# Kernel optimization log

Measured on AMD Instinct MI355X. Metric: run time of the kernel, lower is better.

Reference implementation:

```python
import math
import jax, jax.numpy as jnp
import numpy as np

D_MODEL = 256
NUM_HEAD = 8
NUM_LEVEL = 1
KERNEL = 5
NUM_POINT = KERNEL * KERNEL
NUM_VAR = 5  # with_rotation=True
HEAD_DIM = D_MODEL // NUM_HEAD


def _kernel_indices(k=KERNEL):
    # odd kernel: linspace(-(k-1)/2, (k-1)/2, k); torch.meshgrid default 'ij'; stack([j,i])/k
    idx = jnp.linspace(-(k - 1) / 2.0, (k - 1) / 2.0, k)
    ii, jj = jnp.meshgrid(idx, idx, indexing='ij')
    return jnp.stack([jj, ii], axis=-1).reshape(-1, 2) / k  # (P, 2)


def setup_inputs() -> dict:
    key = jax.random.key(0)
    ks = jax.random.split(key, 8)
    B, LQ = 2, 4096
    Hf, Wf = 188, 188
    LV = Hf * Wf
    d = D_MODEL
    nb = NUM_LEVEL * NUM_HEAD * NUM_VAR
    na = NUM_HEAD * NUM_LEVEL * NUM_POINT
    return {
        'query': jax.random.normal(ks[0], (B, LQ, d), jnp.float32),
        'value': jax.random.normal(ks[1], (B, LV, d), jnp.float32),
        'ref_windows': jax.random.uniform(ks[2], (B, LQ, 7), jnp.float32),
        'W_box': jax.random.normal(ks[3], (nb, d), jnp.float32) * 0.02,
        'b_box': jax.random.uniform(ks[4], (nb,), jnp.float32),
        'W_attn': jax.random.normal(ks[5], (na, d), jnp.float32) * 0.02,
        'b_attn': jnp.zeros((na,), jnp.float32),
        'W_value': jax.random.normal(ks[6], (d, d), jnp.float32) * 0.02,
        'b_value': jnp.zeros((d,), jnp.float32),
        'W_out': jax.random.normal(ks[7], (d, d), jnp.float32) * 0.02,
        'b_out': jnp.zeros((d,), jnp.float32),
        'H_feat': Hf,
        'W_feat': Wf,
    }


def reference(query, value, ref_windows, W_box, b_box, W_attn, b_attn,
              W_value, b_value, W_out, b_out, H_feat, W_feat):
    B, LQ, d = query.shape
    LV = value.shape[1]
    Hh, Lv, P, Dh = NUM_HEAD, NUM_LEVEL, NUM_POINT, HEAD_DIM

    # value projection -> (B, LV, Hh, Dh)
    v = (value @ W_value.T + b_value).reshape(B, LV, Hh, Dh)

    # attention weights: softmax over (level*point) per head
    attn = jax.nn.softmax((query @ W_attn.T + b_attn).reshape(B, LQ, Hh, Lv * P), axis=-1)
    attn = attn.reshape(B, LQ, Hh, Lv, P)

    # --- _where_to_attend ---
    ob = (query @ W_box.T + b_box).reshape(B, LQ, Hh, Lv, NUM_VAR)
    rw = ref_windows[:, :, None, None, :]                    # (B,LQ,1,1,7)
    ref_boxes = rw[..., jnp.array([0, 1, 3, 4])]             # cx, cy, w, h
    ref_angles = rw[..., 6:7]
    off_boxes, off_angles = ob[..., :4], ob[..., 4:5]
    angles = (ref_angles + off_angles / 16.0) * (2.0 * math.pi)
    boxes = ref_boxes + off_boxes / 8.0 * ref_boxes[..., jnp.array([2, 3, 2, 3])]
    center = boxes[..., None, :2]                            # (B,LQ,Hh,Lv,1,2)
    size = boxes[..., None, 2:4]
    cos_a, sin_a = jnp.cos(angles), jnp.sin(angles)
    rot = jnp.stack([cos_a, -sin_a, sin_a, cos_a], axis=-1).reshape(B, LQ, Hh, Lv, 1, 2, 2)
    g = _kernel_indices() * jax.nn.relu(size)                # (B,LQ,Hh,Lv,P,2)
    grid = center + (g[..., None, :] * rot).sum(-1)          # (B,LQ,Hh,Lv,P,2), normalized [0,1]

    # --- single-level bilinear sampling (align_corners=False, zero padding) ---
    gl = grid[:, :, :, 0]                                    # (B,LQ,Hh,P,2)
    gx = gl[..., 0] * W_feat - 0.5
    gy = gl[..., 1] * H_feat - 0.5
    x0 = jnp.floor(gx)
    y0 = jnp.floor(gy)
    x0i = x0.astype(jnp.int32)
    y0i = y0.astype(jnp.int32)
    wx1 = gx - x0
    wy1 = gy - y0
    wx0 = 1.0 - wx1
    wy0 = 1.0 - wy1

    b_idx = jnp.arange(B)[:, None, None, None]
    h_idx = jnp.arange(Hh)[None, None, :, None]

    def gather(yi, xi):
        valid = (xi >= 0) & (xi < W_feat) & (yi >= 0) & (yi < H_feat)
        lin = jnp.clip(yi, 0, H_feat - 1) * W_feat + jnp.clip(xi, 0, W_feat - 1)
        return v[b_idx, lin, h_idx] * valid[..., None]       # (B,LQ,Hh,P,Dh)

    s = (gather(y0i, x0i) * (wy0 * wx0)[..., None]
         + gather(y0i, x0i + 1) * (wy0 * wx1)[..., None]
         + gather(y0i + 1, x0i) * (wy1 * wx0)[..., None]
         + gather(y0i + 1, x0i + 1) * (wy1 * wx1)[..., None])

    out_heads = (s * attn[:, :, :, 0, :, None]).sum(axis=3)  # (B,LQ,Hh,Dh)
    out = out_heads.reshape(B, LQ, Hh * Dh) @ W_out.T + b_out
    attn_w = attn.reshape(B, LQ, Hh, Lv, KERNEL, KERNEL)
    return out, attn_w
```

## Files before the change

kernel.cpp:

```cpp
#include <hip/hip_runtime.h>


typedef float floatx4 __attribute__((ext_vector_type(4)));
typedef short shortx8 __attribute__((ext_vector_type(8)));

#define SB0 __builtin_amdgcn_sched_barrier(0)
#define VMCNT8 asm volatile("s_waitcnt vmcnt(8)" ::: "memory")
#define VMCNT0 asm volatile("s_waitcnt vmcnt(0)" ::: "memory")
#define LGKM0  asm volatile("s_waitcnt lgkmcnt(0)" ::: "memory")

static __device__ __forceinline__ unsigned short f2bf(float x) {
    unsigned int u = __float_as_uint(x);
    return (unsigned short)((u + 0x7fffu + ((u >> 16) & 1u)) >> 16);
}
static __device__ __forceinline__ unsigned int pack2(float a, float b) {
    return (unsigned int)f2bf(a) | ((unsigned int)f2bf(b) << 16);
}
static __device__ __forceinline__ void async16(const void* g, void* lds) {
    __builtin_amdgcn_global_load_lds(
        (const __attribute__((address_space(1))) unsigned int*)g,
        (__attribute__((address_space(3))) unsigned int*)lds, 16, 0, 0);
}

__global__ __launch_bounds__(256) void convert_kernel(
    const float* __restrict__ W_value, unsigned short* __restrict__ wvbf,
    const float* __restrict__ W_attn, const float* __restrict__ W_box,
    float* __restrict__ Wab,
    const float* __restrict__ W_out, unsigned short* __restrict__ wobf,
    const float* __restrict__ b_attn, const float* __restrict__ b_box,
    float* __restrict__ bab)
{
    const int blk = blockIdx.x, tid = threadIdx.x;
    if (blk < 16) {
        int base = blk * 1024 + tid;
#pragma unroll
        for (int k = 0; k < 4; ++k) {
            int j = base + k * 256;
            float4 f = ((const float4*)W_value)[j];
            ((uint2*)wvbf)[j] = make_uint2(pack2(f.x, f.y), pack2(f.z, f.w));
        }
    } else if (blk < 32) {
        int base = (blk - 16) * 1024 + tid;
#pragma unroll
        for (int k = 0; k < 4; ++k) {
            int j = base + k * 256;
            int row = j >> 6, col = (j & 63) * 4;
            float4 f;
            if (row < 200)      f = *(const float4*)(W_attn + (size_t)row * 256 + col);
            else if (row < 240) f = *(const float4*)(W_box + (size_t)(row - 200) * 256 + col);
            else                f = make_float4(0.f, 0.f, 0.f, 0.f);
            ((float4*)Wab)[j] = f;
        }
    } else if (blk < 48) {
        int base = (blk - 32) * 1024 + tid;
#pragma unroll
        for (int k = 0; k < 4; ++k) {
            int j = base + k * 256;
            float4 f = ((const float4*)W_out)[j];
            ((uint2*)wobf)[j] = make_uint2(pack2(f.x, f.y), pack2(f.z, f.w));
        }
    } else {
        bab[tid] = tid < 200 ? b_attn[tid] : (tid < 240 ? b_box[tid - 200] : 0.f);
    }
}

template <int OUTMODE, int AFP32, int BM>
__global__ __launch_bounds__(256) void gemm_bf16(
    const void* __restrict__ Av,
    const unsigned short* __restrict__ Bw,
    const float* __restrict__ bias,
    void* __restrict__ Cv, int M, int LV)
{
    constexpr int NI = BM / 32;
    constexpr int TI = BM / 32;
    __shared__ unsigned short As[2][BM * 64];
    __shared__ unsigned short Bs[2][128 * 64];
    const int tid = threadIdx.x;
    const int wv = tid >> 6, lane = tid & 63;
    const int lr = lane & 15, lq = lane >> 4;
    const int m0 = blockIdx.x * BM, n0 = blockIdx.y * 128;
    const int wm = wv & 1, wn = wv >> 1;
    const int srow = tid >> 3;
    const int colg = tid & 7;
    const int colgSw = colg ^ (srow & 7);
    const int dstA = (srow * 8 + colgSw) * 16;

    floatx4 acc[TI][4];
#pragma unroll
    for (int i = 0; i < TI; ++i)
#pragma unroll
        for (int j = 0; j < 4; ++j) acc[i][j] = (floatx4){0.f, 0.f, 0.f, 0.f};

    auto compute = [&](const unsigned short* Acur, const unsigned short* Bcur) {
#pragma unroll
        for (int kb = 0; kb < 2; ++kb) {
            shortx8 af[TI], bfr[4];
#pragma unroll
            for (int t = 0; t < TI; ++t) {
                int arow = wm * (BM / 2) + t * 16 + lr;
                af[t] = *(const shortx8*)&Acur[arow * 64 + (((kb * 4 + lq) ^ (arow & 7)) * 8)];
            }
#pragma unroll
            for (int t = 0; t < 4; ++t) {
                int brow = wn * 64 + t * 16 + lr;
                bfr[t] = *(const shortx8*)&Bcur[brow * 64 + (((kb * 4 + lq) ^ (brow & 7)) * 8)];
            }
#pragma unroll
            for (int ti = 0; ti < TI; ++ti)
#pragma unroll
                for (int tj = 0; tj < 4; ++tj)
                    acc[ti][tj] = __builtin_amdgcn_mfma_f32_16x16x32_bf16(bfr[tj], af[ti], acc[ti][tj], 0, 0, 0);
        }
    };

    if constexpr (AFP32) {
        const float* Af = (const float*)Av;
        const float* aptr[NI];
#pragma unroll
        for (int i = 0; i < NI; ++i) {
            int ra = m0 + i * 32 + srow; ra = ra < M ? ra : M - 1;
            aptr[i] = Af + (size_t)ra * 256 + colg * 8;
        }
        const unsigned short* bptr = Bw + (size_t)(n0 + srow) * 256 + colgSw * 8;
        float4 ar0[NI], ar1[NI];

#pragma unroll
        for (int i = 0; i < NI; ++i) { ar0[i] = *(const float4*)aptr[i]; ar1[i] = *(const float4*)(aptr[i] + 4); }
#pragma unroll
        for (int i = 0; i < 4; ++i)
            async16(bptr + (size_t)i * 8192, (char*)Bs[0] + i * 4096 + wv * 1024);
        SB0;
#pragma unroll
        for (int i = 0; i < NI; ++i) {
            uint4 pv = make_uint4(pack2(ar0[i].x, ar0[i].y), pack2(ar0[i].z, ar0[i].w),
                                  pack2(ar1[i].x, ar1[i].y), pack2(ar1[i].z, ar1[i].w));
            *(uint4*)((char*)As[0] + i * 4096 + dstA) = pv;
        }
#pragma unroll
        for (int i = 0; i < NI; ++i) { ar0[i] = *(const float4*)(aptr[i] + 64); ar1[i] = *(const float4*)(aptr[i] + 68); }
        SB0;
        VMCNT8;
        LGKM0;
        __builtin_amdgcn_s_barrier();
        SB0;

#pragma unroll
        for (int kc = 0; kc < 4; ++kc) {
            const int cur = kc & 1;
            if (kc < 3) {
#pragma unroll
                for (int i = 0; i < 4; ++i)
                    async16(bptr + (size_t)i * 8192 + (kc + 1) * 64,
                            (char*)Bs[cur ^ 1] + i * 4096 + wv * 1024);
            }
            SB0;
            compute(As[cur], Bs[cur]);
            SB0;
            if (kc < 3) {
#pragma unroll
                for (int i = 0; i < NI; ++i) {
                    uint4 pv = make_uint4(pack2(ar0[i].x, ar0[i].y), pack2(ar0[i].z, ar0[i].w),
                                          pack2(ar1[i].x, ar1[i].y), pack2(ar1[i].z, ar1[i].w));
                    *(uint4*)((char*)As[cur ^ 1] + i * 4096 + dstA) = pv;
                }
                if (kc < 2) {
#pragma unroll
                    for (int i = 0; i < NI; ++i) {
                        ar0[i] = *(const float4*)(aptr[i] + (kc + 2) * 64);
                        ar1[i] = *(const float4*)(aptr[i] + (kc + 2) * 64 + 4);
                    }
                    SB0;
                    VMCNT8;
                } else {
                    SB0;
                    VMCNT0;
                }
                LGKM0;
                __builtin_amdgcn_s_barrier();
                SB0;
            }
        }
    } else {
        const unsigned short* Ab = (const unsigned short*)Av;
#pragma unroll
        for (int i = 0; i < NI; ++i) {
            int ra = m0 + i * 32 + srow; ra = ra < M ? ra : M - 1;
            async16(Ab + (size_t)ra * 256 + colgSw * 8, (char*)As[0] + i * 4096 + wv * 1024);
        }
#pragma unroll
        for (int i = 0; i < 4; ++i) {
            int rb = n0 + i * 32 + srow;
            async16(Bw + (size_t)rb * 256 + colgSw * 8, (char*)Bs[0] + i * 4096 + wv * 1024);
        }
        __syncthreads();
        int cur = 0;
        for (int kc = 0; kc < 4; ++kc) {
            const int nk = (kc + 1) * 64;
            if (kc < 3) {
#pragma unroll
                for (int i = 0; i < NI; ++i) {
                    int ra = m0 + i * 32 + srow; ra = ra < M ? ra : M - 1;
                    async16(Ab + (size_t)ra * 256 + nk + colgSw * 8,
                            (char*)As[cur ^ 1] + i * 4096 + wv * 1024);
                }
#pragma unroll
                for (int i = 0; i < 4; ++i) {
                    int rb = n0 + i * 32 + srow;
                    async16(Bw + (size_t)rb * 256 + nk + colgSw * 8,
                            (char*)Bs[cur ^ 1] + i * 4096 + wv * 1024);
                }
            }
            compute(As[cur], Bs[cur]);
            __syncthreads();
            cur ^= 1;
        }
    }

#pragma unroll
    for (int ti = 0; ti < TI; ++ti) {
        int m = m0 + wm * (BM / 2) + ti * 16 + lr;
        if (m >= M) continue;
        if (OUTMODE == 0) {
            float* Crow = (float*)Cv + (size_t)m * 256;
#pragma unroll
            for (int tj = 0; tj < 4; ++tj) {
                int nb = n0 + wn * 64 + tj * 16 + lq * 4;
                float4 bv = *(const float4*)(bias + nb);
                float4 o = make_float4(acc[ti][tj][0] + bv.x, acc[ti][tj][1] + bv.y,
                                       acc[ti][tj][2] + bv.z, acc[ti][tj][3] + bv.w);
                *(float4*)(Crow + nb) = o;
            }
        } else {
            int b = m >= LV ? 1 : 0;
            int lv = m - (b ? LV : 0);
#pragma unroll
            for (int tj = 0; tj < 4; ++tj) {
                int nb = n0 + wn * 64 + tj * 16 + lq * 4;
                float4 bv = *(const float4*)(bias + nb);
                int h = nb >> 5, dh = nb & 31;
                unsigned short* dst = (unsigned short*)Cv + ((size_t)(b * 8 + h) * LV + lv) * 32 + dh;
                *(uint2*)dst = make_uint2(pack2(acc[ti][tj][0] + bv.x, acc[ti][tj][1] + bv.y),
                                          pack2(acc[ti][tj][2] + bv.z, acc[ti][tj][3] + bv.w));
            }
        }
    }
}

__global__ __launch_bounds__(256) void gemm_nt_bias(
    const float* __restrict__ A, const float* __restrict__ W,
    const float* __restrict__ bias, float* __restrict__ C, int M)
{
    const int K = 256, N = 256;
    __shared__ float As[16][68];
    __shared__ float Bs[16][68];
    int tid = threadIdx.x;
    int tcol = tid & 15, trow = tid >> 4;
    int m0 = blockIdx.x * 64, n0 = blockIdx.y * 64;
    int lr = tid >> 2, lc = (tid & 3) << 2;
    float acc[4][4] = {};
    for (int k0 = 0; k0 < K; k0 += 16) {
        int arow = m0 + lr; if (arow > M - 1) arow = M - 1;
        float4 av = *(const float4*)(A + (size_t)arow * K + k0 + lc);
        float4 wv = *(const float4*)(W + (size_t)(n0 + lr) * K + k0 + lc);
        __syncthreads();
        As[lc + 0][lr] = av.x; As[lc + 1][lr] = av.y; As[lc + 2][lr] = av.z; As[lc + 3][lr] = av.w;
        Bs[lc + 0][lr] = wv.x; Bs[lc + 1][lr] = wv.y; Bs[lc + 2][lr] = wv.z; Bs[lc + 3][lr] = wv.w;
        __syncthreads();
#pragma unroll
        for (int k = 0; k < 16; ++k) {
            float4 a4 = *(const float4*)&As[k][trow << 2];
            float4 b4 = *(const float4*)&Bs[k][tcol << 2];
            float a[4] = {a4.x, a4.y, a4.z, a4.w};
            float bb[4] = {b4.x, b4.y, b4.z, b4.w};
#pragma unroll
            for (int i = 0; i < 4; i++)
#pragma unroll
                for (int j = 0; j < 4; j++) acc[i][j] += a[i] * bb[j];
        }
    }
#pragma unroll
    for (int i = 0; i < 4; i++) {
        int m = m0 + trow * 4 + i;
        if (m >= M) continue;
#pragma unroll
        for (int j = 0; j < 4; j++) {
            int n = n0 + tcol * 4 + j;
            C[(size_t)m * N + n] = acc[i][j] + bias[n];
        }
    }
}

__global__ __launch_bounds__(256) void decode_sample_kernel(
    const unsigned short* __restrict__ v,
    const float* __restrict__ logits,
    const float* __restrict__ ref_windows,
    float* __restrict__ attn_out,
    unsigned short* __restrict__ ohbf,
    const int* __restrict__ Hf_p, const int* __restrict__ Wf_p, int LV, int LQ)
{
    __shared__ float lg[8][32];
    __shared__ float rw[8][7];
    __shared__ float prm[8][6];
    __shared__ float mxinv[8][2];
    __shared__ uint4 pk[8][25][2];

    const int lin = blockIdx.y * 16 + blockIdx.x;
    const int nc = gridDim.y;
    const int seq = lin >> 3;
    const int c = seq % nc;
    const int s = (lin & 7) + ((seq / nc) << 3);
    const int b = s >> 3, h = s & 7;
    const int tid = threadIdx.x;
    const int Hf = *Hf_p, Wf = *Wf_p;
    const size_t mbase = (size_t)b * LQ + c * 8;

    if (tid < 240) {
        int qq = tid / 30, j = tid - qq * 30;
        int col = (j < 25) ? h * 25 + j : 200 + h * 5 + (j - 25);
        lg[qq][j] = logits[(mbase + qq) * 256 + col];
    }
    if (tid < 56) {
        int qq = tid / 7, k = tid - qq * 7;
        rw[qq][k] = ref_windows[(mbase + qq) * 7 + k];
    }
    __syncthreads();

    if (tid < 8) {
        int qq = tid;
        float mx = -1e30f;
#pragma unroll
        for (int p = 0; p < 25; p++) mx = fmaxf(mx, lg[qq][p]);
        float ssum = 0.f;
#pragma unroll
        for (int p = 0; p < 25; p++) ssum += expf(lg[qq][p] - mx);
        mxinv[qq][0] = mx; mxinv[qq][1] = 1.f / ssum;
        float cx = rw[qq][0] + lg[qq][25] * 0.125f * rw[qq][3];
        float cy = rw[qq][1] + lg[qq][26] * 0.125f * rw[qq][4];
        float bw = rw[qq][3] + lg[qq][27] * 0.125f * rw[qq][3];
        float bh = rw[qq][4] + lg[qq][28] * 0.125f * rw[qq][4];
        float ang = (rw[qq][6] + lg[qq][29] * 0.0625f) * 6.283185307179586f;
        prm[qq][0] = cx; prm[qq][1] = cy;
        prm[qq][2] = fmaxf(bw, 0.f); prm[qq][3] = fmaxf(bh, 0.f);
        prm[qq][4] = cosf(ang); prm[qq][5] = sinf(ang);
    }
    __syncthreads();

    if (tid < 200) {
        int qq = tid / 25, p = tid - qq * 25;
        float a = expf(lg[qq][p] - mxinv[qq][0]) * mxinv[qq][1];
        attn_out[(mbase + qq) * 200 + h * 25 + p] = a;
        int pi = p / 5, pj = p - pi * 5;
        float g0 = (float)(pj - 2) * 0.2f * prm[qq][2];
        float g1 = (float)(pi - 2) * 0.2f * prm[qq][3];
        float ca = prm[qq][4], sa = prm[qq][5];
        float gx = (prm[qq][0] + g0 * ca - g1 * sa) * (float)Wf - 0.5f;
        float gy = (prm[qq][1] + g0 * sa + g1 * ca) * (float)Hf - 0.5f;
        float x0f = floorf(gx), y0f = floorf(gy);
        int x0 = (int)x0f, y0 = (int)y0f;
        float wx1 = gx - x0f, wy1 = gy - y0f;
        float wx0 = 1.f - wx1, wy0 = 1.f - wy1;
        int y1 = y0 + 1;
        int bx; float wl, wr;
        if (x0 >= 0 && x0 <= Wf - 2)      { bx = x0;     wl = wx0; wr = wx1; }
        else if (x0 == -1)                { bx = 0;      wl = wx1; wr = 0.f; }
        else if (x0 == Wf - 1)            { bx = Wf - 2; wl = 0.f; wr = wx0; }
        else                              { bx = 0;      wl = 0.f; wr = 0.f; }
        float wy0v = (y0 >= 0 && y0 < Hf) ? wy0 : 0.f;
        float wy1v = (y1 >= 0 && y1 < Hf) ? wy1 : 0.f;
        int cy0 = min(max(y0, 0), Hf - 1), cy1 = min(max(y1, 0), Hf - 1);
        unsigned off0 = (unsigned)(cy0 * Wf + bx) * 16u;
        unsigned off1 = (unsigned)(cy1 * Wf + bx) * 16u;
        float aw0 = a * wy0v, aw1 = a * wy1v;
        pk[qq][p][0] = make_uint4(__float_as_uint(aw0 * wl), __float_as_uint(aw1 * wl), off0, off1);
        pk[qq][p][1] = make_uint4(__float_as_uint(aw0 * wr), __float_as_uint(aw1 * wr), off0, off1);
    }
    __syncthreads();

    const int qq = tid >> 5, l = tid & 31;
    const unsigned int* vw = (const unsigned int*)(v + (size_t)s * LV * 32);
    const uint4* pkp = &pk[qq][0][l >> 4];
    float e0 = 0.f, o0 = 0.f, e1 = 0.f, o1 = 0.f;
#pragma unroll
    for (int p = 0; p < 25; ++p) {
        uint4 t = pkp[2 * p];
        float w0 = __uint_as_float(t.x), w1 = __uint_as_float(t.y);
        unsigned u0 = vw[t.z + l];
        unsigned u1 = vw[t.w + l];
        e0 += w0 * __uint_as_float(u0 << 16);
        o0 += w0 * __uint_as_float(u0 & 0xffff0000u);
        e1 += w1 * __uint_as_float(u1 << 16);
        o1 += w1 * __uint_as_float(u1 & 0xffff0000u);
    }
    float a0 = e0 + e1, a1 = o0 + o1;
    a0 += __shfl_xor(a0, 16, 32);
    a1 += __shfl_xor(a1, 16, 32);
    if (l < 16)
        ((unsigned int*)ohbf)[(mbase + qq) * 128 + h * 16 + l] = pack2(a0, a1);
}

extern "C" void kernel_launch(void* const* d_in, const int* in_sizes, int n_in,
                              void* d_out, int out_size, void* d_ws, size_t ws_size,
                              hipStream_t stream) {
    const float* query       = (const float*)d_in[0];
    const float* value       = (const float*)d_in[1];
    const float* ref_windows = (const float*)d_in[2];
    const float* W_box       = (const float*)d_in[3];
    const float* b_box       = (const float*)d_in[4];
    const float* W_attn      = (const float*)d_in[5];
    const float* b_attn      = (const float*)d_in[6];
    const float* W_value     = (const float*)d_in[7];
    const float* b_value     = (const float*)d_in[8];
    const float* W_out       = (const float*)d_in[9];
    const float* b_out       = (const float*)d_in[10];
    const int*   Hf          = (const int*)d_in[11];
    const int*   Wf          = (const int*)d_in[12];

    const int M1 = in_sizes[1] / 256;
    const int MQ = in_sizes[0] / 256;
    const int LQ = MQ / 2;
    const int LV = M1 / 2;

    unsigned short* Vout = (unsigned short*)d_ws;
    unsigned short* ohbf = Vout + (size_t)M1 * 256;
    unsigned short* wvbf = ohbf + (size_t)MQ * 256;
    unsigned short* wobf = wvbf + 65536;
    float* Wab       = (float*)(wobf + 65536);
    float* bab       = Wab + 65536;
    float* logits    = bab + 256;

    float* out0     = (float*)d_out;
    float* attn_out = out0 + (size_t)MQ * 256;

    convert_kernel<<<49, 256, 0, stream>>>(W_value, wvbf, W_attn, W_box, Wab,
                                           W_out, wobf, b_attn, b_box, bab);
    dim3 g1((M1 + 127) / 128, 2);
    gemm_bf16<1, 1, 128><<<g1, 256, 0, stream>>>(value, wvbf, b_value, Vout, M1, LV);
    dim3 g2(MQ / 64, 4);
    gemm_nt_bias<<<g2, 256, 0, stream>>>(query, Wab, bab, logits, MQ);
    decode_sample_kernel<<<dim3(16, LQ / 8), 256, 0, stream>>>(
        Vout, logits, ref_windows, attn_out, ohbf, Hf, Wf, LV, LQ);
    dim3 g4(MQ / 64, 2);
    gemm_bf16<0, 0, 64><<<g4, 256, 0, stream>>>(ohbf, wobf, b_out, out0, MQ, LV);
}
```

Measured before the change: 212.4 us.

## Fuse value and query projection GEMMs into one interleaved launch

```diff
diff --git a/kernel.cpp b/kernel.cpp
--- a/kernel.cpp
+++ b/kernel.cpp
@@ -64,80 +64,87 @@
     }
 }
 
-template <int OUTMODE, int AFP32, int BM>
-__global__ __launch_bounds__(256) void gemm_bf16(
-    const void* __restrict__ Av,
-    const unsigned short* __restrict__ Bw,
-    const float* __restrict__ bias,
-    void* __restrict__ Cv, int M, int LV)
+__global__ __launch_bounds__(256) void fused_proj(
+    const float* __restrict__ value,
+    const unsigned short* __restrict__ wvbf,
+    const float* __restrict__ b_value,
+    unsigned short* __restrict__ Vout, int M1, int LV,
+    const float* __restrict__ query,
+    const float* __restrict__ Wab,
+    const float* __restrict__ bab,
+    float* __restrict__ logits, int MQ)
 {
-    constexpr int NI = BM / 32;
-    constexpr int TI = BM / 32;
-    __shared__ unsigned short As[2][BM * 64];
-    __shared__ unsigned short Bs[2][128 * 64];
+    __shared__ char smem[65536];
+    const int f = blockIdx.x;
     const int tid = threadIdx.x;
-    const int wv = tid >> 6, lane = tid & 63;
-    const int lr = lane & 15, lq = lane >> 4;
-    const int m0 = blockIdx.x * BM, n0 = blockIdx.y * 128;
-    const int wm = wv & 1, wn = wv >> 1;
-    const int srow = tid >> 3;
-    const int colg = tid & 7;
-    const int colgSw = colg ^ (srow & 7);
-    const int dstA = (srow * 8 + colgSw) * 16;
-
-    floatx4 acc[TI][4];
-#pragma unroll
-    for (int i = 0; i < TI; ++i)
-#pragma unroll
-        for (int j = 0; j < 4; ++j) acc[i][j] = (floatx4){0.f, 0.f, 0.f, 0.f};
-
-    auto compute = [&](const unsigned short* Acur, const unsigned short* Bcur) {
-#pragma unroll
-        for (int kb = 0; kb < 2; ++kb) {
-            shortx8 af[TI], bfr[4];
-#pragma unroll
-            for (int t = 0; t < TI; ++t) {
-                int arow = wm * (BM / 2) + t * 16 + lr;
-                af[t] = *(const shortx8*)&Acur[arow * 64 + (((kb * 4 + lq) ^ (arow & 7)) * 8)];
-            }
-#pragma unroll
-            for (int t = 0; t < 4; ++t) {
-                int brow = wn * 64 + t * 16 + lr;
-                bfr[t] = *(const shortx8*)&Bcur[brow * 64 + (((kb * 4 + lq) ^ (brow & 7)) * 8)];
-            }
-#pragma unroll
-            for (int ti = 0; ti < TI; ++ti)
-#pragma unroll
-                for (int tj = 0; tj < 4; ++tj)
-                    acc[ti][tj] = __builtin_amdgcn_mfma_f32_16x16x32_bf16(bfr[tj], af[ti], acc[ti][tj], 0, 0, 0);
-        }
-    };
-
-    if constexpr (AFP32) {
-        const float* Af = (const float*)Av;
-        const float* aptr[NI];
-#pragma unroll
-        for (int i = 0; i < NI; ++i) {
+    const bool isK2 = (f % 3 == 2) && (f < 1536);
+
+    if (!isK2) {
+        const int k1id = f - ((f < 1536) ? ((f + 1) / 3) : 512);
+        const int bx = k1id % 553, by = k1id / 553;
+        unsigned short* AsL = (unsigned short*)smem;
+        unsigned short* BsL = (unsigned short*)smem + 16384;
+        const int wv = tid >> 6, lane = tid & 63;
+        const int lr = lane & 15, lq = lane >> 4;
+        const int m0 = bx * 128, n0 = by * 128;
+        const int wm = wv & 1, wn = wv >> 1;
+        const int srow = tid >> 3;
+        const int colg = tid & 7;
+        const int colgSw = colg ^ (srow & 7);
+        const int dstA = (srow * 8 + colgSw) * 16;
+        const int M = M1;
+
+        floatx4 acc[4][4];
+#pragma unroll
+        for (int i = 0; i < 4; ++i)
+#pragma unroll
+            for (int j = 0; j < 4; ++j) acc[i][j] = (floatx4){0.f, 0.f, 0.f, 0.f};
+
+        auto compute = [&](const unsigned short* Acur, const unsigned short* Bcur) {
+#pragma unroll
+            for (int kb = 0; kb < 2; ++kb) {
+                shortx8 af[4], bfr[4];
+#pragma unroll
+                for (int t = 0; t < 4; ++t) {
+                    int arow = wm * 64 + t * 16 + lr;
+                    af[t] = *(const shortx8*)&Acur[arow * 64 + (((kb * 4 + lq) ^ (arow & 7)) * 8)];
+                }
+#pragma unroll
+                for (int t = 0; t < 4; ++t) {
+                    int brow = wn * 64 + t * 16 + lr;
+                    bfr[t] = *(const shortx8*)&Bcur[brow * 64 + (((kb * 4 + lq) ^ (brow & 7)) * 8)];
+                }
+#pragma unroll
+                for (int ti = 0; ti < 4; ++ti)
+#pragma unroll
+                    for (int tj = 0; tj < 4; ++tj)
+                        acc[ti][tj] = __builtin_amdgcn_mfma_f32_16x16x32_bf16(bfr[tj], af[ti], acc[ti][tj], 0, 0, 0);
+            }
+        };
+
+        const float* aptr[4];
+#pragma unroll
+        for (int i = 0; i < 4; ++i) {
             int ra = m0 + i * 32 + srow; ra = ra < M ? ra : M - 1;
-            aptr[i] = Af + (size_t)ra * 256 + colg * 8;
-        }
-        const unsigned short* bptr = Bw + (size_t)(n0 + srow) * 256 + colgSw * 8;
-        float4 ar0[NI], ar1[NI];
-
-#pragma unroll
-        for (int i = 0; i < NI; ++i) { ar0[i] = *(const float4*)aptr[i]; ar1[i] = *(const float4*)(aptr[i] + 4); }
+            aptr[i] = value + (size_t)ra * 256 + colg * 8;
+        }
+        const unsigned short* bptr = wvbf + (size_t)(n0 + srow) * 256 + colgSw * 8;
+        float4 ar0[4], ar1[4];
+
+#pragma unroll
+        for (int i = 0; i < 4; ++i) { ar0[i] = *(const float4*)aptr[i]; ar1[i] = *(const float4*)(aptr[i] + 4); }
 #pragma unroll
         for (int i = 0; i < 4; ++i)
-            async16(bptr + (size_t)i * 8192, (char*)Bs[0] + i * 4096 + wv * 1024);
+            async16(bptr + (size_t)i * 8192, (char*)BsL + i * 4096 + wv * 1024);
         SB0;
 #pragma unroll
-        for (int i = 0; i < NI; ++i) {
+        for (int i = 0; i < 4; ++i) {
             uint4 pv = make_uint4(pack2(ar0[i].x, ar0[i].y), pack2(ar0[i].z, ar0[i].w),
                                   pack2(ar1[i].x, ar1[i].y), pack2(ar1[i].z, ar1[i].w));
-            *(uint4*)((char*)As[0] + i * 4096 + dstA) = pv;
-        }
-#pragma unroll
-        for (int i = 0; i < NI; ++i) { ar0[i] = *(const float4*)(aptr[i] + 64); ar1[i] = *(const float4*)(aptr[i] + 68); }
+            *(uint4*)((char*)AsL + i * 4096 + dstA) = pv;
+        }
+#pragma unroll
+        for (int i = 0; i < 4; ++i) { ar0[i] = *(const float4*)(aptr[i] + 64); ar1[i] = *(const float4*)(aptr[i] + 68); }
         SB0;
         VMCNT8;
         LGKM0;
@@ -147,25 +154,29 @@
 #pragma unroll
         for (int kc = 0; kc < 4; ++kc) {
             const int cur = kc & 1;
+            unsigned short* Acur = AsL + cur * 8192;
+            unsigned short* Anxt = AsL + (cur ^ 1) * 8192;
+            unsigned short* Bcur = BsL + cur * 8192;
+            unsigned short* Bnxt = BsL + (cur ^ 1) * 8192;
             if (kc < 3) {
 #pragma unroll
                 for (int i = 0; i < 4; ++i)
                     async16(bptr + (size_t)i * 8192 + (kc + 1) * 64,
-                            (char*)Bs[cur ^ 1] + i * 4096 + wv * 1024);
+                            (char*)Bnxt + i * 4096 + wv * 1024);
             }
             SB0;
-            compute(As[cur], Bs[cur]);
+            compute(Acur, Bcur);
             SB0;
             if (kc < 3) {
 #pragma unroll
-                for (int i = 0; i < NI; ++i) {
+                for (int i = 0; i < 4; ++i) {
                     uint4 pv = make_uint4(pack2(ar0[i].x, ar0[i].y), pack2(ar0[i].z, ar0[i].w),
                                           pack2(ar1[i].x, ar1[i].y), pack2(ar1[i].z, ar1[i].w));
-                    *(uint4*)((char*)As[cur ^ 1] + i * 4096 + dstA) = pv;
+                    *(uint4*)((char*)Anxt + i * 4096 + dstA) = pv;
                 }
                 if (kc < 2) {
 #pragma unroll
-                    for (int i = 0; i < NI; ++i) {
+                    for (int i = 0; i < 4; ++i) {
                         ar0[i] = *(const float4*)(aptr[i] + (kc + 2) * 64);
                         ar1[i] = *(const float4*)(aptr[i] + (kc + 2) * 64 + 4);
                     }
@@ -180,112 +191,157 @@
                 SB0;
             }
         }
+#pragma unroll
+        for (int ti = 0; ti < 4; ++ti) {
+            int m = m0 + wm * 64 + ti * 16 + lr;
+            if (m >= M) continue;
+            int b = m >= LV ? 1 : 0;
+            int lv = m - (b ? LV : 0);
+#pragma unroll
+            for (int tj = 0; tj < 4; ++tj) {
+                int nb = n0 + wn * 64 + tj * 16 + lq * 4;
+                float4 bv = *(const float4*)(b_value + nb);
+                int h = nb >> 5, dh = nb & 31;
+                unsigned short* dst = Vout + ((size_t)(b * 8 + h) * LV + lv) * 32 + dh;
+                *(uint2*)dst = make_uint2(pack2(acc[ti][tj][0] + bv.x, acc[ti][tj][1] + bv.y),
+                                          pack2(acc[ti][tj][2] + bv.z, acc[ti][tj][3] + bv.w));
+            }
+        }
     } else {
-        const unsigned short* Ab = (const unsigned short*)Av;
-#pragma unroll
-        for (int i = 0; i < NI; ++i) {
-            int ra = m0 + i * 32 + srow; ra = ra < M ? ra : M - 1;
-            async16(Ab + (size_t)ra * 256 + colgSw * 8, (char*)As[0] + i * 4096 + wv * 1024);
-        }
-#pragma unroll
-        for (int i = 0; i < 4; ++i) {
-            int rb = n0 + i * 32 + srow;
-            async16(Bw + (size_t)rb * 256 + colgSw * 8, (char*)Bs[0] + i * 4096 + wv * 1024);
-        }
+        const int id = f / 3;
+        const int m0 = (id & 127) * 64, n0 = (id >> 7) * 64;
+        const int K = 256, N = 256, M = MQ;
+        float* As2 = (float*)smem;
+        float* Bs2 = (float*)smem + 16 * 68;
+        int tcol = tid & 15, trow = tid >> 4;
+        int lr = tid >> 2, lc = (tid & 3) << 2;
+        float acc[4][4] = {};
+        for (int k0 = 0; k0 < K; k0 += 16) {
+            int arow = m0 + lr; if (arow > M - 1) arow = M - 1;
+            float4 av = *(const float4*)(query + (size_t)arow * K + k0 + lc);
+            float4 wv = *(const float4*)(Wab + (size_t)(n0 + lr) * K + k0 + lc);
+            __syncthreads();
+            As2[(lc + 0) * 68 + lr] = av.x; As2[(lc + 1) * 68 + lr] = av.y;
+            As2[(lc + 2) * 68 + lr] = av.z; As2[(lc + 3) * 68 + lr] = av.w;
+            Bs2[(lc + 0) * 68 + lr] = wv.x; Bs2[(lc + 1) * 68 + lr] = wv.y;
+            Bs2[(lc + 2) * 68 + lr] = wv.z; Bs2[(lc + 3) * 68 + lr] = wv.w;
+            __syncthreads();
+#pragma unroll
+            for (int k = 0; k < 16; ++k) {
+                float4 a4 = *(const float4*)&As2[k * 68 + (trow << 2)];
+                float4 b4 = *(const float4*)&Bs2[k * 68 + (tcol << 2)];
+                float a[4] = {a4.x, a4.y, a4.z, a4.w};
+                float bb[4] = {b4.x, b4.y, b4.z, b4.w};
+#pragma unroll
+                for (int i = 0; i < 4; i++)
+#pragma unroll
+                    for (int j = 0; j < 4; j++) acc[i][j] += a[i] * bb[j];
+            }
+        }
+#pragma unroll
+        for (int i = 0; i < 4; i++) {
+            int m = m0 + trow * 4 + i;
+            if (m >= M) continue;
+#pragma unroll
+            for (int j = 0; j < 4; j++) {
+                int n = n0 + tcol * 4 + j;
+                logits[(size_t)m * N + n] = acc[i][j] + bab[n];
+            }
+        }
+    }
+}
+
+__global__ __launch_bounds__(256) void gemm_out(
+    const unsigned short* __restrict__ Ab,
+    const unsigned short* __restrict__ Bw,
+    const float* __restrict__ bias,
+    float* __restrict__ C, int M)
+{
+    constexpr int BM = 64;
+    constexpr int NI = BM / 32, TI = BM / 32;
+    __shared__ unsigned short As[2][BM * 64];
+    __shared__ unsigned short Bs[2][128 * 64];
+    const int tid = threadIdx.x;
+    const int wv = tid >> 6, lane = tid & 63;
+    const int lr = lane & 15, lq = lane >> 4;
+    const int m0 = blockIdx.x * BM, n0 = blockIdx.y * 128;
+    const int wm = wv & 1, wn = wv >> 1;
+    const int srow = tid >> 3;
+    const int colg = tid & 7;
+    const int colgSw = colg ^ (srow & 7);
+
+    floatx4 acc[TI][4];
+#pragma unroll
+    for (int i = 0; i < TI; ++i)
+#pragma unroll
+        for (int j = 0; j < 4; ++j) acc[i][j] = (floatx4){0.f, 0.f, 0.f, 0.f};
+
+    auto compute = [&](const unsigned short* Acur, const unsigned short* Bcur) {
+#pragma unroll
+        for (int kb = 0; kb < 2; ++kb) {
+            shortx8 af[TI], bfr[4];
+#pragma unroll
+            for (int t = 0; t < TI; ++t) {
+                int arow = wm * (BM / 2) + t * 16 + lr;
+                af[t] = *(const shortx8*)&Acur[arow * 64 + (((kb * 4 + lq) ^ (arow & 7)) * 8)];
+            }
+#pragma unroll
+            for (int t = 0; t < 4; ++t) {
+                int brow = wn * 64 + t * 16 + lr;
+                bfr[t] = *(const shortx8*)&Bcur[brow * 64 + (((kb * 4 + lq) ^ (brow & 7)) * 8)];
+            }
+#pragma unroll
+            for (int ti = 0; ti < TI; ++ti)
+#pragma unroll
+                for (int tj = 0; tj < 4; ++tj)
+                    acc[ti][tj] = __builtin_amdgcn_mfma_f32_16x16x32_bf16(bfr[tj], af[ti], acc[ti][tj], 0, 0, 0);
+        }
+    };
+
+#pragma unroll
+    for (int i = 0; i < NI; ++i) {
+        int ra = m0 + i * 32 + srow; ra = ra < M ? ra : M - 1;
+        async16(Ab + (size_t)ra * 256 + colgSw * 8, (char*)As[0] + i * 4096 + wv * 1024);
+    }
+#pragma unroll
+    for (int i = 0; i < 4; ++i) {
+        int rb = n0 + i * 32 + srow;
+        async16(Bw + (size_t)rb * 256 + colgSw * 8, (char*)Bs[0] + i * 4096 + wv * 1024);
+    }
+    __syncthreads();
+    int cur = 0;
+    for (int kc = 0; kc < 4; ++kc) {
+        const int nk = (kc + 1) * 64;
+        if (kc < 3) {
+#pragma unroll
+            for (int i = 0; i < NI; ++i) {
+                int ra = m0 + i * 32 + srow; ra = ra < M ? ra : M - 1;
+                async16(Ab + (size_t)ra * 256 + nk + colgSw * 8,
+                        (char*)As[cur ^ 1] + i * 4096 + wv * 1024);
+            }
+#pragma unroll
+            for (int i = 0; i < 4; ++i) {
+                int rb = n0 + i * 32 + srow;
+                async16(Bw + (size_t)rb * 256 + nk + colgSw * 8,
+                        (char*)Bs[cur ^ 1] + i * 4096 + wv * 1024);
+            }
+        }
+        compute(As[cur], Bs[cur]);
         __syncthreads();
-        int cur = 0;
-        for (int kc = 0; kc < 4; ++kc) {
-            const int nk = (kc + 1) * 64;
-            if (kc < 3) {
-#pragma unroll
-                for (int i = 0; i < NI; ++i) {
-                    int ra = m0 + i * 32 + srow; ra = ra < M ? ra : M - 1;
-                    async16(Ab + (size_t)ra * 256 + nk + colgSw * 8,
-                            (char*)As[cur ^ 1] + i * 4096 + wv * 1024);
-                }
-#pragma unroll
-                for (int i = 0; i < 4; ++i) {
-                    int rb = n0 + i * 32 + srow;
-                    async16(Bw + (size_t)rb * 256 + nk + colgSw * 8,
-                            (char*)Bs[cur ^ 1] + i * 4096 + wv * 1024);
-                }
-            }
-            compute(As[cur], Bs[cur]);
-            __syncthreads();
-            cur ^= 1;
-        }
-    }
-
+        cur ^= 1;
+    }
 #pragma unroll
     for (int ti = 0; ti < TI; ++ti) {
         int m = m0 + wm * (BM / 2) + ti * 16 + lr;
         if (m >= M) continue;
-        if (OUTMODE == 0) {
-            float* Crow = (float*)Cv + (size_t)m * 256;
-#pragma unroll
-            for (int tj = 0; tj < 4; ++tj) {
-                int nb = n0 + wn * 64 + tj * 16 + lq * 4;
-                float4 bv = *(const float4*)(bias + nb);
-                float4 o = make_float4(acc[ti][tj][0] + bv.x, acc[ti][tj][1] + bv.y,
-                                       acc[ti][tj][2] + bv.z, acc[ti][tj][3] + bv.w);
-                *(float4*)(Crow + nb) = o;
-            }
-        } else {
-            int b = m >= LV ? 1 : 0;
-            int lv = m - (b ? LV : 0);
-#pragma unroll
-            for (int tj = 0; tj < 4; ++tj) {
-                int nb = n0 + wn * 64 + tj * 16 + lq * 4;
-                float4 bv = *(const float4*)(bias + nb);
-                int h = nb >> 5, dh = nb & 31;
-                unsigned short* dst = (unsigned short*)Cv + ((size_t)(b * 8 + h) * LV + lv) * 32 + dh;
-                *(uint2*)dst = make_uint2(pack2(acc[ti][tj][0] + bv.x, acc[ti][tj][1] + bv.y),
-                                          pack2(acc[ti][tj][2] + bv.z, acc[ti][tj][3] + bv.w));
-            }
-        }
-    }
-}
-
-__global__ __launch_bounds__(256) void gemm_nt_bias(
-    const float* __restrict__ A, const float* __restrict__ W,
-    const float* __restrict__ bias, float* __restrict__ C, int M)
-{
-    const int K = 256, N = 256;
-    __shared__ float As[16][68];
-    __shared__ float Bs[16][68];
-    int tid = threadIdx.x;
-    int tcol = tid & 15, trow = tid >> 4;
-    int m0 = blockIdx.x * 64, n0 = blockIdx.y * 64;
-    int lr = tid >> 2, lc = (tid & 3) << 2;
-    float acc[4][4] = {};
-    for (int k0 = 0; k0 < K; k0 += 16) {
-        int arow = m0 + lr; if (arow > M - 1) arow = M - 1;
-        float4 av = *(const float4*)(A + (size_t)arow * K + k0 + lc);
-        float4 wv = *(const float4*)(W + (size_t)(n0 + lr) * K + k0 + lc);
-        __syncthreads();
-        As[lc + 0][lr] = av.x; As[lc + 1][lr] = av.y; As[lc + 2][lr] = av.z; As[lc + 3][lr] = av.w;
-        Bs[lc + 0][lr] = wv.x; Bs[lc + 1][lr] = wv.y; Bs[lc + 2][lr] = wv.z; Bs[lc + 3][lr] = wv.w;
-        __syncthreads();
-#pragma unroll
-        for (int k = 0; k < 16; ++k) {
-            float4 a4 = *(const float4*)&As[k][trow << 2];
-            float4 b4 = *(const float4*)&Bs[k][tcol << 2];
-            float a[4] = {a4.x, a4.y, a4.z, a4.w};
-            float bb[4] = {b4.x, b4.y, b4.z, b4.w};
-#pragma unroll
-            for (int i = 0; i < 4; i++)
-#pragma unroll
-                for (int j = 0; j < 4; j++) acc[i][j] += a[i] * bb[j];
-        }
-    }
-#pragma unroll
-    for (int i = 0; i < 4; i++) {
-        int m = m0 + trow * 4 + i;
-        if (m >= M) continue;
-#pragma unroll
-        for (int j = 0; j < 4; j++) {
-            int n = n0 + tcol * 4 + j;
-            C[(size_t)m * N + n] = acc[i][j] + bias[n];
+        float* Crow = C + (size_t)m * 256;
+#pragma unroll
+        for (int tj = 0; tj < 4; ++tj) {
+            int nb = n0 + wn * 64 + tj * 16 + lq * 4;
+            float4 bv = *(const float4*)(bias + nb);
+            float4 o = make_float4(acc[ti][tj][0] + bv.x, acc[ti][tj][1] + bv.y,
+                                   acc[ti][tj][2] + bv.z, acc[ti][tj][3] + bv.w);
+            *(float4*)(Crow + nb) = o;
         }
     }
 }
@@ -433,12 +489,10 @@
 
     convert_kernel<<<49, 256, 0, stream>>>(W_value, wvbf, W_attn, W_box, Wab,
                                            W_out, wobf, b_attn, b_box, bab);
-    dim3 g1((M1 + 127) / 128, 2);
-    gemm_bf16<1, 1, 128><<<g1, 256, 0, stream>>>(value, wvbf, b_value, Vout, M1, LV);
-    dim3 g2(MQ / 64, 4);
-    gemm_nt_bias<<<g2, 256, 0, stream>>>(query, Wab, bab, logits, MQ);
+    fused_proj<<<1618, 256, 0, stream>>>(value, wvbf, b_value, Vout, M1, LV,
+                                         query, Wab, bab, logits, MQ);
     decode_sample_kernel<<<dim3(16, LQ / 8), 256, 0, stream>>>(
         Vout, logits, ref_windows, attn_out, ohbf, Hf, Wf, LV, LQ);
     dim3 g4(MQ / 64, 2);
-    gemm_bf16<0, 0, 64><<<g4, 256, 0, stream>>>(ohbf, wobf, b_out, out0, MQ, LV);
-}
+    gemm_out<<<g4, 256, 0, stream>>>(ohbf, wobf, b_out, out0, MQ);
+}
```

Result: slower. 229.1 us (+7.9%).
